# Kernel optimization log

Measured on AMD Instinct MI355X. Metric: run time of the kernel, lower is better.

The kernel has to match this reference:

```python
import jax, jax.numpy as jnp
import numpy as np

COST_CLASS = 1.0
COST_GIOU = 1.0
MAXV = 8  # max vertices of intersection of two convex quads


def _corners(box):  # (5,) -> (4,2) CCW corners of rotated box (cx,cy,w,h,theta)
    cx, cy, w, h, t = box[0], box[1], box[2], box[3], box[4]
    c, s = jnp.cos(t), jnp.sin(t)
    dx = jnp.array([-0.5, 0.5, 0.5, -0.5], box.dtype) * w
    dy = jnp.array([-0.5, -0.5, 0.5, 0.5], box.dtype) * h
    x = cx + dx * c - dy * s
    y = cy + dx * s + dy * c
    return jnp.stack([x, y], axis=-1)


def _poly_area(poly, cnt):  # shoelace on masked vertex buffer (MAXV,2)
    idx = jnp.arange(MAXV)
    valid = idx < cnt
    nxt = jnp.where(idx + 1 < cnt, idx + 1, 0)
    cr = poly[:, 0] * poly[nxt, 1] - poly[nxt, 0] * poly[:, 1]
    return 0.5 * jnp.abs(jnp.sum(jnp.where(valid, cr, 0.0)))


def _clip(carry, edge):  # Sutherland-Hodgman clip of masked polygon by halfplane left of edge a->b
    poly, cnt = carry
    a, b = edge[0], edge[1]
    d = b - a
    idx = jnp.arange(MAXV)
    valid = idx < cnt
    nxt_i = jnp.where(idx + 1 < cnt, idx + 1, 0)
    cur, nxt = poly, poly[nxt_i]
    s_cur = d[0] * (cur[:, 1] - a[1]) - d[1] * (cur[:, 0] - a[0])
    s_nxt = d[0] * (nxt[:, 1] - a[1]) - d[1] * (nxt[:, 0] - a[0])
    in_cur, in_nxt = s_cur >= 0, s_nxt >= 0
    den = s_cur - s_nxt
    den = jnp.where(jnp.abs(den) > 1e-9, den, 1e-9)
    ipt = cur + (s_cur / den)[:, None] * (nxt - cur)
    pts = jnp.stack([cur, ipt], 1).reshape(2 * MAXV, 2)
    msk = jnp.stack([valid & in_cur, valid & (in_cur ^ in_nxt)], 1).reshape(2 * MAXV)
    pos = jnp.where(msk, jnp.cumsum(msk) - 1, 2 * MAXV)
    new_poly = jnp.zeros((MAXV, 2), poly.dtype).at[pos].set(pts, mode='drop')
    return (new_poly, jnp.sum(msk).astype(cnt.dtype)), None


def _inter_area(cs, cc):  # intersection area of two convex quads (4,2),(4,2)
    poly0 = jnp.zeros((MAXV, 2), cs.dtype).at[:4].set(cs)
    edges = jnp.stack([cc, jnp.roll(cc, -1, axis=0)], axis=1)  # (4,2,2)
    (poly, cnt), _ = jax.lax.scan(_clip, (poly0, jnp.asarray(4, jnp.int32)), edges)
    return _poly_area(poly, cnt)


def _giou_cost(bt, bp):  # cal_giou(target, pred) ~= 1 - rotated GIoU
    ct, cp = _corners(bt), _corners(bp)
    inter = _inter_area(cp, ct)
    union = bt[2] * bt[3] + bp[2] * bp[3] - inter
    allc = jnp.concatenate([ct, cp], 0)
    enc = (allc[:, 0].max() - allc[:, 0].min()) * (allc[:, 1].max() - allc[:, 1].min())
    giou = inter / union - (enc - union) / enc
    return 1.0 - giou


def _costs(p_box, p_score, t_box, t_score):
    # p_box [B,M,5], t_box [B,N,5] with M >= N (m>n branch: zero-padded extra cols)
    B, M, _ = p_box.shape
    N = t_box.shape[1]
    box = jax.vmap(
        lambda pb, tb: jax.vmap(lambda bp: jax.vmap(lambda bt: _giou_cost(bt, bp))(tb))(pb)
    )(p_box, t_box)  # [B,M,N]
    score = jnp.maximum(0.0, t_score[:, None, :] - p_score[:, :, None])  # [B,M,N]
    pad = ((0, 0), (0, 0), (0, M - N))
    score_p = jnp.pad(score, pad)
    box_p = jnp.pad(box, pad)
    cost = COST_CLASS * score_p + COST_GIOU * box_p
    return cost, score_p, box_p

_costs_j = jax.jit(_costs)


def _lsa(cost):  # Hungarian (Jonker-Volgenant style, e-maxx), square cost matrix
    cost = np.asarray(cost, dtype=np.float64)
    n = cost.shape[0]
    INF = 1e30
    u = np.zeros(n + 1)
    v = np.zeros(n + 1)
    p = np.zeros(n + 1, dtype=np.int64)
    way = np.zeros(n + 1, dtype=np.int64)
    for i in range(1, n + 1):
        p[0] = i
        j0 = 0
        minv = np.full(n + 1, INF)
        used = np.zeros(n + 1, dtype=bool)
        while True:
            used[j0] = True
            i0 = p[j0]
            cur = cost[i0 - 1] - u[i0] - v[1:]
            free = ~used[1:]
            upd = free & (cur < minv[1:])
            minv[1:][upd] = cur[upd]
            way[1:][upd] = j0
            mv = np.where(free, minv[1:], INF)
            j0 = int(np.argmin(mv)) + 1
            delta = mv[j0 - 1]
            u[p[used]] += delta
            v[used] -= delta
            minv[1:][free] -= delta
            if p[j0] == 0:
                break
        while j0 != 0:
            j1 = way[j0]
            p[j0] = p[j1]
            j0 = j1
    cols = np.zeros(n, dtype=np.int64)
    for j in range(1, n + 1):
        cols[p[j] - 1] = j - 1
    return np.arange(n), cols


def setup_inputs() -> dict:
    key = jax.random.key(0)
    ks = jax.random.split(key, 6)
    B, M, N = 4, 256, 192

    def boxes(k1, k2, k3, n):
        c = jax.random.uniform(k1, (B, n, 2), minval=-50.0, maxval=50.0)
        wh = jax.random.uniform(k2, (B, n, 2), minval=1.0, maxval=5.0)
        ang = jax.random.uniform(k3, (B, n, 1), minval=-np.pi, maxval=np.pi)
        return jnp.concatenate([c, wh, ang], -1).astype(jnp.float32)

    return {
        'pred_rot_box': boxes(ks[0], ks[1], ks[2], M),
        'pred_score': jax.random.uniform(jax.random.fold_in(key, 10), (B, M), dtype=jnp.float32),
        'target_rot_box': boxes(ks[3], ks[4], ks[5], N),
        'target_score': jax.random.uniform(jax.random.fold_in(key, 11), (B, N), dtype=jnp.float32),
    }


def reference(pred_rot_box, pred_score, target_rot_box, target_score):
    cost, score_p, box_p = _costs_j(pred_rot_box, pred_score, target_rot_box, target_score)
    B = cost.shape[0]
    N = target_rot_box.shape[1]
    cost_np = np.asarray(cost)
    score_np = np.asarray(score_p)
    box_np = np.asarray(box_p)
    match, msc, mbc = [], [], []
    for b in range(B):
        r, c = _lsa(cost_np[b])
        match.append(cost_np[b][r, c].sum() / N)
        msc.append(score_np[b][r, c].sum() / N)
        mbc.append(box_np[b][r, c].sum() / N)
    return jnp.asarray(np.stack([match, msc, mbc]), dtype=jnp.float32)  # [3, B]
```

## Files before the change

### kernel.cpp

```cpp
#include <hip/hip_runtime.h>
#include <cmath>

#define MAXV 8

__global__ __launch_bounds__(256) void cost_kernel(
    const float* __restrict__ p_box, const float* __restrict__ p_score,
    const float* __restrict__ t_box, const float* __restrict__ t_score,
    float* __restrict__ Ct, float* __restrict__ boxc,
    int B, int M, int N)
{
    int g = blockIdx.x * 256 + threadIdx.x;
    int total = B * M * N;
    if (g >= total) return;
    int b = g / (M * N);
    int rem = g - b * M * N;
    int n = rem / M;
    int m = rem - n * M;

    const float* bp = p_box + ((size_t)b * M + m) * 5;
    const float* bt = t_box + ((size_t)b * N + n) * 5;
    float pcx = bp[0], pcy = bp[1], pw = bp[2], ph = bp[3], pth = bp[4];
    float tcx = bt[0], tcy = bt[1], tw = bt[2], th = bt[3], tth = bt[4];

    float pc = cosf(pth), ps = sinf(pth);
    float tc = cosf(tth), ts = sinf(tth);

    const float DX[4] = {-0.5f, 0.5f, 0.5f, -0.5f};
    const float DY[4] = {-0.5f, -0.5f, 0.5f, 0.5f};
    float cpx[4], cpy[4], ctx[4], cty[4];
#pragma unroll
    for (int k = 0; k < 4; k++) {
        float dx = DX[k] * pw, dy = DY[k] * ph;
        cpx[k] = pcx + dx * pc - dy * ps;
        cpy[k] = pcy + dx * ps + dy * pc;
        float dx2 = DX[k] * tw, dy2 = DY[k] * th;
        ctx[k] = tcx + dx2 * tc - dy2 * ts;
        cty[k] = tcy + dx2 * ts + dy2 * tc;
    }

    float px[MAXV], py[MAXV];
#pragma unroll
    for (int k = 0; k < MAXV; k++) {
        px[k] = (k < 4) ? cpx[k] : 0.0f;
        py[k] = (k < 4) ? cpy[k] : 0.0f;
    }
    int cnt = 4;

#pragma unroll
    for (int e = 0; e < 4; e++) {
        float ax = ctx[e], ay = cty[e];
        float bx2 = ctx[(e + 1) & 3], by2 = cty[(e + 1) & 3];
        float dx = bx2 - ax, dy = by2 - ay;
        float qx[MAXV], qy[MAXV];
#pragma unroll
        for (int k = 0; k < MAXV; k++) { qx[k] = 0.0f; qy[k] = 0.0f; }
        int nc = 0;
#pragma unroll
        for (int i = 0; i < MAXV; i++) {
            if (i < cnt) {
                bool wrap = !(i + 1 < cnt);
                float nx = wrap ? px[0] : px[(i + 1) & 7];
                float ny = wrap ? py[0] : py[(i + 1) & 7];
                float sc = dx * (py[i] - ay) - dy * (px[i] - ax);
                float sn = dx * (ny - ay) - dy * (nx - ax);
                bool inc = (sc >= 0.0f), inn = (sn >= 0.0f);
                float den = sc - sn;
                if (!(fabsf(den) > 1e-9f)) den = 1e-9f;
                float t = sc / den;
                float ix = px[i] + t * (nx - px[i]);
                float iy = py[i] + t * (ny - py[i]);
                if (inc) {
                    if (nc < MAXV) { qx[nc] = px[i]; qy[nc] = py[i]; }
                    nc++;
                }
                if (inc != inn) {
                    if (nc < MAXV) { qx[nc] = ix; qy[nc] = iy; }
                    nc++;
                }
            }
        }
        cnt = (nc > MAXV) ? MAXV : nc;
#pragma unroll
        for (int k = 0; k < MAXV; k++) {
            px[k] = (k < cnt) ? qx[k] : 0.0f;
            py[k] = (k < cnt) ? qy[k] : 0.0f;
        }
    }

    float a2 = 0.0f;
#pragma unroll
    for (int i = 0; i < MAXV; i++) {
        if (i < cnt) {
            bool wrap = !(i + 1 < cnt);
            float nx = wrap ? px[0] : px[(i + 1) & 7];
            float ny = wrap ? py[0] : py[(i + 1) & 7];
            a2 += px[i] * ny - nx * py[i];
        }
    }
    float inter = 0.5f * fabsf(a2);

    float uni = tw * th + pw * ph - inter;

    float xmin = ctx[0], xmax = ctx[0], ymin = cty[0], ymax = cty[0];
#pragma unroll
    for (int k = 1; k < 4; k++) {
        xmin = fminf(xmin, ctx[k]); xmax = fmaxf(xmax, ctx[k]);
        ymin = fminf(ymin, cty[k]); ymax = fmaxf(ymax, cty[k]);
    }
#pragma unroll
    for (int k = 0; k < 4; k++) {
        xmin = fminf(xmin, cpx[k]); xmax = fmaxf(xmax, cpx[k]);
        ymin = fminf(ymin, cpy[k]); ymax = fmaxf(ymax, cpy[k]);
    }
    float enc = (xmax - xmin) * (ymax - ymin);

    float giou = inter / uni - (enc - uni) / enc;
    float bc = 1.0f - giou;
    float scst = fmaxf(0.0f, t_score[b * N + n] - p_score[b * M + m]);

    Ct[((size_t)b * N + n) * M + m] = scst + bc;
    boxc[((size_t)b * M + m) * N + n] = bc;
}

__global__ __launch_bounds__(64) void rowmin_kernel(
    const float* __restrict__ Ct, float* __restrict__ rmv, int M)
{
    int bt = blockIdx.x;
    int lane = threadIdx.x;
    const float* row = Ct + (size_t)bt * M;

    float bv = 1e30f;
    for (int c = 4 * lane; c < M; c += 256) {
        float4 v = *reinterpret_cast<const float4*>(row + c);
        bv = fminf(bv, fminf(fminf(v.x, v.y), fminf(v.z, v.w)));
    }
#pragma unroll
    for (int off = 1; off < 64; off <<= 1)
        bv = fminf(bv, __shfl_xor(bv, off, 64));
    if (lane == 0) rmv[bt] = bv;
}

__global__ __launch_bounds__(256) void colmin_kernel(
    const float* __restrict__ Ct, const float* __restrict__ rmv,
    float* __restrict__ vmin, int* __restrict__ varg, int M, int N)
{
    int b = blockIdx.x;
    const float* Cb = Ct + (size_t)b * N * M;
    const float* rb = rmv + (size_t)b * N;
    for (int j = threadIdx.x; j < M; j += blockDim.x) {
        float bv = 1e30f; int bt = 0;
        for (int t = 0; t < N; ++t) {
            float val = Cb[(size_t)t * M + j] - rb[t];
            if (val < bv) { bv = val; bt = t; }
        }
        vmin[(size_t)b * M + j] = bv;
        varg[(size_t)b * M + j] = bt + 1;
    }
}

__device__ __forceinline__ int sel4(int a0, int a1, int a2, int a3, int s) {
    return s == 0 ? a0 : (s == 1 ? a1 : (s == 2 ? a2 : a3));
}

#define DPP_FMIN32_STAGE(val, CTRL) do {                                      \
    int _o = __builtin_amdgcn_update_dpp(0x7F800000,                          \
                 __float_as_int(val), CTRL, 0xf, 0xf, false);                 \
    (val) = fminf((val), __int_as_float(_o));                                 \
} while (0)

#define DPP_PAIR_STAGE(g1, g2, CTRL) do {                                     \
    int _b1 = __builtin_amdgcn_update_dpp(0x7F800000,                         \
                  __float_as_int(g1), CTRL, 0xf, 0xf, false);                 \
    int _b2 = __builtin_amdgcn_update_dpp(0x7F800000,                         \
                  __float_as_int(g2), CTRL, 0xf, 0xf, false);                 \
    float _o1 = __int_as_float(_b1), _o2 = __int_as_float(_b2);               \
    float _n2 = fminf(fmaxf((g1), _o1), fminf((g2), _o2));                    \
    (g1) = fminf((g1), _o1);                                                  \
    (g2) = _n2;                                                               \
} while (0)

__global__ __launch_bounds__(64) void hungarian_rect(
    const float* __restrict__ Ct, const float* __restrict__ boxc,
    const float* __restrict__ p_score, const float* __restrict__ t_score,
    const float* __restrict__ rmv, const float* __restrict__ vmin,
    const int* __restrict__ varg,
    float* __restrict__ out, int B, int M, int N)
{
    const float FINF = 1e30f;
    const int IINF = 0x7fffffff;
    int b = blockIdx.x;
    int lane = threadIdx.x;
    const float* C = Ct + (size_t)b * N * M;

    __shared__ float u[257];
    __shared__ int claim[257];
    __shared__ int ulist[257];
    __shared__ int dlist[257];

    {
        int total = N * M;
        for (int off = 4 * lane; off < total; off += 256) {
            float4 w = *reinterpret_cast<const float4*>(C + off);
            asm volatile("" :: "v"(w.x), "v"(w.y), "v"(w.z), "v"(w.w));
        }
    }

    for (int k = lane; k < N; k += 64) u[k + 1] = rmv[b * N + k];
    for (int k = lane; k < 257; k += 64) claim[k] = IINF;
    __syncthreads();

    const int j_base = 4 * lane + 1;
    float v0, v1, v2, v3;
    int va0, va1, va2, va3;
    {
        const float4 vm = *reinterpret_cast<const float4*>(
            vmin + (size_t)b * M + 4 * lane);
        v0 = vm.x; v1 = vm.y; v2 = vm.z; v3 = vm.w;
        const int4 vg = *reinterpret_cast<const int4*>(
            varg + (size_t)b * M + 4 * lane);
        va0 = vg.x; va1 = vg.y; va2 = vg.z; va3 = vg.w;
    }

    float m0, m1, m2, m3;
    int p0 = 0, p1 = 0, p2 = 0, p3 = 0;
    int w0 = 0, w1 = 0, w2 = 0, w3 = 0;

    atomicMin(&claim[va0], j_base + 0);
    atomicMin(&claim[va1], j_base + 1);
    atomicMin(&claim[va2], j_base + 2);
    atomicMin(&claim[va3], j_base + 3);
    __syncthreads();
    p0 = (claim[va0] == j_base + 0) ? va0 : 0;
    p1 = (claim[va1] == j_base + 1) ? va1 : 0;
    p2 = (claim[va2] == j_base + 2) ? va2 : 0;
    p3 = (claim[va3] == j_base + 3) ? va3 : 0;

    int ucnt = 0;
    for (int c0 = 0; c0 < N; c0 += 64) {
        int t = c0 + lane + 1;
        bool un = (t <= N) && (claim[t] == IINF);
        unsigned long long mask = __ballot(un);
        int pos = ucnt + __popcll(mask & ((1ULL << lane) - 1ULL));
        if (un) ulist[pos] = t;
        ucnt += (int)__popcll(mask);
    }
    __syncthreads();

    int dcnt = 0;
    {
        int pi = 0, steps = 0;
        int i = (pi < ucnt) ? ulist[pi++] : 0;
        while (i != 0) {
            ++steps;
            if (steps > 2048) {
                if (lane == 0) dlist[dcnt] = i;
                dcnt++;
                while (pi < ucnt) {
                    if (lane == 0) dlist[dcnt] = ulist[pi];
                    dcnt++; pi++;
                }
                break;
            }
            float4 r4 = *reinterpret_cast<const float4*>(
                C + (size_t)(i - 1) * M + 4 * lane);
            float rc0 = r4.x - v0, rc1 = r4.y - v1;
            float rc2 = r4.z - v2, rc3 = r4.w - v3;
            float l1 = rc0; int s1 = 0;
            if (rc1 < l1) { l1 = rc1; s1 = 1; }
            if (rc2 < l1) { l1 = rc2; s1 = 2; }
            if (rc3 < l1) { l1 = rc3; s1 = 3; }
            float l2 = FINF;
            if (s1 != 0) l2 = fminf(l2, rc0);
            if (s1 != 1) l2 = fminf(l2, rc1);
            if (s1 != 2) l2 = fminf(l2, rc2);
            if (s1 != 3) l2 = fminf(l2, rc3);

            float g1 = l1, g2 = l2;
            DPP_PAIR_STAGE(g1, g2, 0x111);
            DPP_PAIR_STAGE(g1, g2, 0x112);
            DPP_PAIR_STAGE(g1, g2, 0x114);
            DPP_PAIR_STAGE(g1, g2, 0x118);
            DPP_PAIR_STAGE(g1, g2, 0x142);
            DPP_PAIR_STAGE(g1, g2, 0x143);
            float u1 = __int_as_float(
                __builtin_amdgcn_readlane(__float_as_int(g1), 63));
            float u2 = __int_as_float(
                __builtin_amdgcn_readlane(__float_as_int(g2), 63));
            unsigned long long ball = __ballot(l1 == u1);
            int owner = __builtin_ctzll(ball);
            int pk = (j_base + s1) | (sel4(p0, p1, p2, p3, s1) << 9);
            pk = __builtin_amdgcn_readlane(pk, owner);
            int j1 = pk & 511, k = pk >> 9;

            if (u1 < u2) {
                if (lane == 0) u[i] = u2;
                if (lane == ((j1 - 1) >> 2)) {
                    int s = (j1 - 1) & 3;
                    float dv = u2 - u1;
                    if (s == 0) { v0 -= dv; p0 = i; }
                    else if (s == 1) { v1 -= dv; p1 = i; }
                    else if (s == 2) { v2 -= dv; p2 = i; }
                    else { v3 -= dv; p3 = i; }
                }
                if (k > 0) { i = k; continue; }
            } else if (k == 0) {
                if (lane == 0) u[i] = u1;
                if (lane == ((j1 - 1) >> 2)) {
                    int s = (j1 - 1) & 3;
                    if (s == 0) p0 = i;
                    else if (s == 1) p1 = i;
                    else if (s == 2) p2 = i;
                    else p3 = i;
                }
            } else {
                if (lane == 0) { u[i] = u1; dlist[dcnt] = i; }
                dcnt++;
            }
            i = (pi < ucnt) ? ulist[pi++] : 0;
        }
    }
    __syncthreads();

    for (int uk = 0; uk < dcnt; ++uk) {
        int t = dlist[uk];
        m0 = FINF; m1 = FINF; m2 = FINF; m3 = FINF;
        int usedm = 0;
        float ur0 = 0, ur1 = 0, ur2 = 0, ur3 = 0;
        int tg0 = 0, tg1 = 0, tg2 = 0, tg3 = 0;
        int j0 = 0;
        int icur = t;
        float ut = u[t];
        float u0 = ut;
        float4 r4 = *reinterpret_cast<const float4*>(
            C + (size_t)(t - 1) * M + 4 * lane);
        int jn;

        while (true) {
            if (j0 != 0 && ((j0 - 1) >> 2) == lane) {
                int s = (j0 - 1) & 3;
                usedm |= 1 << s;
                if (s == 0) { ur0 = u0; tg0 = icur; }
                else if (s == 1) { ur1 = u0; tg1 = icur; }
                else if (s == 2) { ur2 = u0; tg2 = icur; }
                else { ur3 = u0; tg3 = icur; }
            }

            float a0 = FINF, a1 = FINF, a2f = FINF, a3 = FINF;
            if (!(usedm & 1)) {
                float cur = (r4.x - u0) - v0;
                if (cur < m0) { m0 = cur; w0 = j0; }
                a0 = m0;
            }
            if (!(usedm & 2)) {
                float cur = (r4.y - u0) - v1;
                if (cur < m1) { m1 = cur; w1 = j0; }
                a1 = m1;
            }
            if (!(usedm & 4)) {
                float cur = (r4.z - u0) - v2;
                if (cur < m2) { m2 = cur; w2 = j0; }
                a2f = m2;
            }
            if (!(usedm & 8)) {
                float cur = (r4.w - u0) - v3;
                if (cur < m3) { m3 = cur; w3 = j0; }
                a3 = m3;
            }

            float av = a0; int sa = 0;
            if (a1 < av)  { av = a1;  sa = 1; }
            if (a2f < av) { av = a2f; sa = 2; }
            if (a3 < av)  { av = a3;  sa = 3; }

            float wv_ = av;
            DPP_FMIN32_STAGE(wv_, 0x111);
            DPP_FMIN32_STAGE(wv_, 0x112);
            DPP_FMIN32_STAGE(wv_, 0x114);
            DPP_FMIN32_STAGE(wv_, 0x118);
            DPP_FMIN32_STAGE(wv_, 0x142);
            DPP_FMIN32_STAGE(wv_, 0x143);
            float delta = __int_as_float(
                __builtin_amdgcn_readlane(__float_as_int(wv_), 63));

            unsigned long long ball = __ballot(av == delta);
            int owner = __builtin_ctzll(ball);
            int pk = (j_base + sa) | (sel4(p0, p1, p2, p3, sa) << 9);
            pk = __builtin_amdgcn_readlane(pk, owner);
            int jn_ = pk & 511, pjn = pk >> 9;

            int nxt = (pjn > 0) ? pjn : t;
            float u_next = u[nxt];
            float4 r4n = *reinterpret_cast<const float4*>(
                C + (size_t)(nxt - 1) * M + 4 * lane);

            if (usedm & 1) { ur0 += delta; v0 -= delta; } else m0 -= delta;
            if (usedm & 2) { ur1 += delta; v1 -= delta; } else m1 -= delta;
            if (usedm & 4) { ur2 += delta; v2 -= delta; } else m2 -= delta;
            if (usedm & 8) { ur3 += delta; v3 -= delta; } else m3 -= delta;
            ut += delta;

            jn = jn_;
            if (pjn == 0) break;
            j0 = jn_; u0 = u_next; r4 = r4n; icur = pjn;
        }

        if (usedm & 1) u[tg0] = ur0;
        if (usedm & 2) u[tg1] = ur1;
        if (usedm & 4) u[tg2] = ur2;
        if (usedm & 8) u[tg3] = ur3;
        if (lane == 0) u[t] = ut;

        int jj = jn, prev = 0;
        while (true) {
            int idx = jj - 1;
            int o = idx >> 2, s = idx & 3;
            int packv = sel4(w0, w1, w2, w3, s) |
                        (sel4(p0, p1, p2, p3, s) << 9);
            packv = __builtin_amdgcn_readlane(packv, o);
            int wv = packv & 511, pold = packv >> 9;
            if (prev != 0) {
                int pi = prev - 1;
                if (lane == (pi >> 2)) {
                    int sp = pi & 3;
                    if (sp == 0) p0 = pold;
                    else if (sp == 1) p1 = pold;
                    else if (sp == 2) p2 = pold;
                    else p3 = pold;
                }
            }
            if (wv == 0) {
                if (lane == o) {
                    if (s == 0) p0 = t;
                    else if (s == 1) p1 = t;
                    else if (s == 2) p2 = t;
                    else p3 = t;
                }
                break;
            }
            prev = jj; jj = wv;
        }
    }

    double sm = 0.0, ss = 0.0, sb = 0.0;
#pragma unroll
    for (int s = 0; s < 4; ++s) {
        int pt = sel4(p0, p1, p2, p3, s);
        if (pt != 0) {
            int r = j_base + s - 1;
            int c = pt - 1;
            sm += (double)C[(size_t)c * M + r];
            sb += (double)boxc[((size_t)b * M + r) * N + c];
            ss += (double)fmaxf(0.0f, t_score[b * N + c] - p_score[b * M + r]);
        }
    }
#pragma unroll
    for (int off = 1; off < 64; off <<= 1) {
        sm += __shfl_xor(sm, off, 64);
        ss += __shfl_xor(ss, off, 64);
        sb += __shfl_xor(sb, off, 64);
    }
    if (lane == 0) {
        out[0 * B + b] = (float)(sm / N);
        out[1 * B + b] = (float)(ss / N);
        out[2 * B + b] = (float)(sb / N);
    }
}

extern "C" void kernel_launch(void* const* d_in, const int* in_sizes, int n_in,
                              void* d_out, int out_size, void* d_ws, size_t ws_size,
                              hipStream_t stream) {
    int B = out_size / 3;
    int M = in_sizes[1] / B;
    int N = in_sizes[3] / B;

    const float* p_box   = (const float*)d_in[0];
    const float* p_score = (const float*)d_in[1];
    const float* t_box   = (const float*)d_in[2];
    const float* t_score = (const float*)d_in[3];
    float* out = (float*)d_out;

    float* Ct   = (float*)d_ws;
    float* boxc = Ct + (size_t)B * N * M;
    float* rmv  = boxc + (size_t)B * M * N;
    float* vmin = rmv + (size_t)B * N;
    int*   varg = (int*)(vmin + (size_t)B * M);

    int total = B * M * N;
    cost_kernel<<<(total + 255) / 256, 256, 0, stream>>>(
        p_box, p_score, t_box, t_score, Ct, boxc, B, M, N);
    rowmin_kernel<<<B * N, 64, 0, stream>>>(Ct, rmv, M);
    colmin_kernel<<<B, 256, 0, stream>>>(Ct, rmv, vmin, varg, M, N);
    hungarian_rect<<<B, 64, 0, stream>>>(
        Ct, boxc, p_score, t_score, rmv, vmin, varg, out, B, M, N);
}
```

Before: 230.2 us.

## Replace sequential augmenting row reduction with parallel auction-style bidding rounds

The serial augmenting row reduction in the Hungarian kernel, which handled one row per step using wave-wide DPP reductions, is replaced by up to 64 rounds of auction-style bidding. In each round every unassigned row scans its full cost row against prices held in LDS and finds its best and second-best columns. It then bids for its best column through a 64-bit atomicMax, and each winning column updates its owner and price. Each lane now reads whole rows serially instead of the wave cooperating on one row, which costs more memory traffic per row. The result could also differ from the old order and leave more rows for the later shortest-path augmentation phase.

```diff
diff --git a/kernel.cpp b/kernel.cpp
--- a/kernel.cpp
+++ b/kernel.cpp
@@ -168,17 +168,6 @@
     (val) = fminf((val), __int_as_float(_o));                                 \
 } while (0)
 
-#define DPP_PAIR_STAGE(g1, g2, CTRL) do {                                     \
-    int _b1 = __builtin_amdgcn_update_dpp(0x7F800000,                         \
-                  __float_as_int(g1), CTRL, 0xf, 0xf, false);                 \
-    int _b2 = __builtin_amdgcn_update_dpp(0x7F800000,                         \
-                  __float_as_int(g2), CTRL, 0xf, 0xf, false);                 \
-    float _o1 = __int_as_float(_b1), _o2 = __int_as_float(_b2);               \
-    float _n2 = fminf(fmaxf((g1), _o1), fminf((g2), _o2));                    \
-    (g1) = fminf((g1), _o1);                                                  \
-    (g2) = _n2;                                                               \
-} while (0)
-
 __global__ __launch_bounds__(64) void hungarian_rect(
     const float* __restrict__ Ct, const float* __restrict__ boxc,
     const float* __restrict__ p_score, const float* __restrict__ t_score,
@@ -193,8 +182,12 @@
     const float* C = Ct + (size_t)b * N * M;
 
     __shared__ float u[257];
+    __shared__ float v_lds[256];
+    __shared__ int colOwner[256];
+    __shared__ int rowMatch[257];
     __shared__ int claim[257];
-    __shared__ int ulist[257];
+    __shared__ unsigned long long bid[256];
+    __shared__ int rlist[257];
     __shared__ int dlist[257];
 
     {
@@ -206,120 +199,121 @@
     }
 
     for (int k = lane; k < N; k += 64) u[k + 1] = rmv[b * N + k];
-    for (int k = lane; k < 257; k += 64) claim[k] = IINF;
+    for (int k = lane; k < 257; k += 64) { claim[k] = IINF; rowMatch[k] = 0; }
     __syncthreads();
 
     const int j_base = 4 * lane + 1;
-    float v0, v1, v2, v3;
     int va0, va1, va2, va3;
     {
         const float4 vm = *reinterpret_cast<const float4*>(
             vmin + (size_t)b * M + 4 * lane);
-        v0 = vm.x; v1 = vm.y; v2 = vm.z; v3 = vm.w;
+        v_lds[4 * lane + 0] = vm.x; v_lds[4 * lane + 1] = vm.y;
+        v_lds[4 * lane + 2] = vm.z; v_lds[4 * lane + 3] = vm.w;
         const int4 vg = *reinterpret_cast<const int4*>(
             varg + (size_t)b * M + 4 * lane);
         va0 = vg.x; va1 = vg.y; va2 = vg.z; va3 = vg.w;
     }
-
-    float m0, m1, m2, m3;
-    int p0 = 0, p1 = 0, p2 = 0, p3 = 0;
-    int w0 = 0, w1 = 0, w2 = 0, w3 = 0;
 
     atomicMin(&claim[va0], j_base + 0);
     atomicMin(&claim[va1], j_base + 1);
     atomicMin(&claim[va2], j_base + 2);
     atomicMin(&claim[va3], j_base + 3);
     __syncthreads();
-    p0 = (claim[va0] == j_base + 0) ? va0 : 0;
-    p1 = (claim[va1] == j_base + 1) ? va1 : 0;
-    p2 = (claim[va2] == j_base + 2) ? va2 : 0;
-    p3 = (claim[va3] == j_base + 3) ? va3 : 0;
-
-    int ucnt = 0;
+    {
+        int own0 = (claim[va0] == j_base + 0) ? va0 : 0;
+        int own1 = (claim[va1] == j_base + 1) ? va1 : 0;
+        int own2 = (claim[va2] == j_base + 2) ? va2 : 0;
+        int own3 = (claim[va3] == j_base + 3) ? va3 : 0;
+        colOwner[4 * lane + 0] = own0; if (own0) rowMatch[own0] = j_base + 0;
+        colOwner[4 * lane + 1] = own1; if (own1) rowMatch[own1] = j_base + 1;
+        colOwner[4 * lane + 2] = own2; if (own2) rowMatch[own2] = j_base + 2;
+        colOwner[4 * lane + 3] = own3; if (own3) rowMatch[own3] = j_base + 3;
+    }
+    __syncthreads();
+
+    for (int round = 0; round < 64; ++round) {
+        int rcnt = 0;
+        for (int c0 = 0; c0 < N; c0 += 64) {
+            int t = c0 + lane + 1;
+            bool un = (t <= N) && (rowMatch[t] == 0);
+            unsigned long long mask = __ballot(un);
+            int pos = rcnt + (int)__popcll(mask & ((1ULL << lane) - 1ULL));
+            if (un) rlist[pos] = t;
+            rcnt += (int)__popcll(mask);
+        }
+        if (rcnt == 0) break;
+        for (int j = lane; j < M; j += 64) bid[j] = 0ULL;
+        __syncthreads();
+
+        for (int c0 = 0; c0 < rcnt; c0 += 64) {
+            int t = (c0 + lane < rcnt) ? rlist[c0 + lane] : 0;
+            if (t) {
+                const float* row = C + (size_t)(t - 1) * M;
+                float mn1 = FINF, mn2 = FINF; int j1 = 0;
+                for (int jj = 0; jj < M; jj += 4) {
+                    float4 c4 = *reinterpret_cast<const float4*>(row + jj);
+                    float rc;
+                    rc = c4.x - v_lds[jj];
+                    if (rc < mn1) { mn2 = mn1; mn1 = rc; j1 = jj; }
+                    else mn2 = fminf(mn2, rc);
+                    rc = c4.y - v_lds[jj + 1];
+                    if (rc < mn1) { mn2 = mn1; mn1 = rc; j1 = jj + 1; }
+                    else mn2 = fminf(mn2, rc);
+                    rc = c4.z - v_lds[jj + 2];
+                    if (rc < mn1) { mn2 = mn1; mn1 = rc; j1 = jj + 2; }
+                    else mn2 = fminf(mn2, rc);
+                    rc = c4.w - v_lds[jj + 3];
+                    if (rc < mn1) { mn2 = mn1; mn1 = rc; j1 = jj + 3; }
+                    else mn2 = fminf(mn2, rc);
+                }
+                float dv = mn2 - mn1;
+                if (dv == 0.0f && colOwner[j1] != 0) {
+                    rowMatch[t] = -1;
+                } else {
+                    u[t] = mn2;
+                    unsigned long long pk =
+                        ((unsigned long long)(unsigned)__float_as_int(dv) << 32)
+                        | (unsigned)t;
+                    atomicMax(&bid[j1], pk);
+                }
+            }
+        }
+        __syncthreads();
+
+#pragma unroll
+        for (int s = 0; s < 4; ++s) {
+            int j = 4 * lane + s;
+            unsigned long long bk = bid[j];
+            if (bk) {
+                int r = (int)(unsigned)(bk & 0xffffffffULL);
+                float dv = __int_as_float((int)(bk >> 32));
+                int old = colOwner[j];
+                colOwner[j] = r;
+                rowMatch[r] = j + 1;
+                if (old) rowMatch[old] = 0;
+                v_lds[j] -= dv;
+            }
+        }
+        __syncthreads();
+    }
+
+    int dcnt = 0;
     for (int c0 = 0; c0 < N; c0 += 64) {
         int t = c0 + lane + 1;
-        bool un = (t <= N) && (claim[t] == IINF);
-        unsigned long long mask = __ballot(un);
-        int pos = ucnt + __popcll(mask & ((1ULL << lane) - 1ULL));
-        if (un) ulist[pos] = t;
-        ucnt += (int)__popcll(mask);
+        bool dd = (t <= N) && (rowMatch[t] <= 0);
+        unsigned long long mask = __ballot(dd);
+        int pos = dcnt + (int)__popcll(mask & ((1ULL << lane) - 1ULL));
+        if (dd) dlist[pos] = t;
+        dcnt += (int)__popcll(mask);
     }
     __syncthreads();
 
-    int dcnt = 0;
-    {
-        int pi = 0, steps = 0;
-        int i = (pi < ucnt) ? ulist[pi++] : 0;
-        while (i != 0) {
-            ++steps;
-            if (steps > 2048) {
-                if (lane == 0) dlist[dcnt] = i;
-                dcnt++;
-                while (pi < ucnt) {
-                    if (lane == 0) dlist[dcnt] = ulist[pi];
-                    dcnt++; pi++;
-                }
-                break;
-            }
-            float4 r4 = *reinterpret_cast<const float4*>(
-                C + (size_t)(i - 1) * M + 4 * lane);
-            float rc0 = r4.x - v0, rc1 = r4.y - v1;
-            float rc2 = r4.z - v2, rc3 = r4.w - v3;
-            float l1 = rc0; int s1 = 0;
-            if (rc1 < l1) { l1 = rc1; s1 = 1; }
-            if (rc2 < l1) { l1 = rc2; s1 = 2; }
-            if (rc3 < l1) { l1 = rc3; s1 = 3; }
-            float l2 = FINF;
-            if (s1 != 0) l2 = fminf(l2, rc0);
-            if (s1 != 1) l2 = fminf(l2, rc1);
-            if (s1 != 2) l2 = fminf(l2, rc2);
-            if (s1 != 3) l2 = fminf(l2, rc3);
-
-            float g1 = l1, g2 = l2;
-            DPP_PAIR_STAGE(g1, g2, 0x111);
-            DPP_PAIR_STAGE(g1, g2, 0x112);
-            DPP_PAIR_STAGE(g1, g2, 0x114);
-            DPP_PAIR_STAGE(g1, g2, 0x118);
-            DPP_PAIR_STAGE(g1, g2, 0x142);
-            DPP_PAIR_STAGE(g1, g2, 0x143);
-            float u1 = __int_as_float(
-                __builtin_amdgcn_readlane(__float_as_int(g1), 63));
-            float u2 = __int_as_float(
-                __builtin_amdgcn_readlane(__float_as_int(g2), 63));
-            unsigned long long ball = __ballot(l1 == u1);
-            int owner = __builtin_ctzll(ball);
-            int pk = (j_base + s1) | (sel4(p0, p1, p2, p3, s1) << 9);
-            pk = __builtin_amdgcn_readlane(pk, owner);
-            int j1 = pk & 511, k = pk >> 9;
-
-            if (u1 < u2) {
-                if (lane == 0) u[i] = u2;
-                if (lane == ((j1 - 1) >> 2)) {
-                    int s = (j1 - 1) & 3;
-                    float dv = u2 - u1;
-                    if (s == 0) { v0 -= dv; p0 = i; }
-                    else if (s == 1) { v1 -= dv; p1 = i; }
-                    else if (s == 2) { v2 -= dv; p2 = i; }
-                    else { v3 -= dv; p3 = i; }
-                }
-                if (k > 0) { i = k; continue; }
-            } else if (k == 0) {
-                if (lane == 0) u[i] = u1;
-                if (lane == ((j1 - 1) >> 2)) {
-                    int s = (j1 - 1) & 3;
-                    if (s == 0) p0 = i;
-                    else if (s == 1) p1 = i;
-                    else if (s == 2) p2 = i;
-                    else p3 = i;
-                }
-            } else {
-                if (lane == 0) { u[i] = u1; dlist[dcnt] = i; }
-                dcnt++;
-            }
-            i = (pi < ucnt) ? ulist[pi++] : 0;
-        }
-    }
-    __syncthreads();
+    float v0 = v_lds[4 * lane + 0], v1 = v_lds[4 * lane + 1];
+    float v2 = v_lds[4 * lane + 2], v3 = v_lds[4 * lane + 3];
+    int p0 = colOwner[4 * lane + 0], p1 = colOwner[4 * lane + 1];
+    int p2 = colOwner[4 * lane + 2], p3 = colOwner[4 * lane + 3];
+    int w0 = 0, w1 = 0, w2 = 0, w3 = 0;
+    float m0, m1, m2, m3;
 
     for (int uk = 0; uk < dcnt; ++uk) {
         int t = dlist[uk];
```

Result: slower. 622.0 us (+170.2%).

## Switch Hungarian duals to double and add reduction-transfer and zero-delta auction steps

Applied to the files above, without the earlier changes.

Moves the dual potentials, column minima and warp reductions in the Hungarian solver from float to double, using split 32-bit DPP moves for the 64-bit min reductions. After the initial column-claim assignment it adds a reduction-transfer step that tightens the duals of assigned rows. It also lets the greedy augmenting phase take a few extra zero-slack reassignment steps per row, so fewer rows fall through to the expensive shortest-path loop. The FP64 arithmetic and doubled DPP traffic make each step of the serial loop costlier, and the rmv pointer cast to double may be misaligned for odd sizes.

```diff
diff --git a/kernel.cpp b/kernel.cpp
--- a/kernel.cpp
+++ b/kernel.cpp
@@ -142,15 +142,15 @@
 
 __global__ __launch_bounds__(256) void colmin_kernel(
     const float* __restrict__ Ct, const float* __restrict__ rmv,
-    float* __restrict__ vmin, int* __restrict__ varg, int M, int N)
+    double* __restrict__ vmin, int* __restrict__ varg, int M, int N)
 {
     int b = blockIdx.x;
     const float* Cb = Ct + (size_t)b * N * M;
     const float* rb = rmv + (size_t)b * N;
     for (int j = threadIdx.x; j < M; j += blockDim.x) {
-        float bv = 1e30f; int bt = 0;
+        double bv = 1e30; int bt = 0;
         for (int t = 0; t < N; ++t) {
-            float val = Cb[(size_t)t * M + j] - rb[t];
+            double val = (double)Cb[(size_t)t * M + j] - (double)rb[t];
             if (val < bv) { bv = val; bt = t; }
         }
         vmin[(size_t)b * M + j] = bv;
@@ -162,40 +162,60 @@
     return s == 0 ? a0 : (s == 1 ? a1 : (s == 2 ? a2 : a3));
 }
 
-#define DPP_FMIN32_STAGE(val, CTRL) do {                                      \
-    int _o = __builtin_amdgcn_update_dpp(0x7F800000,                          \
-                 __float_as_int(val), CTRL, 0xf, 0xf, false);                 \
-    (val) = fminf((val), __int_as_float(_o));                                 \
+#define DPP_FMIN64_STAGE(val, CTRL) do {                                      \
+    long long _bits = __double_as_longlong(val);                              \
+    int _lo = __builtin_amdgcn_update_dpp(0, (int)_bits,                      \
+                                          CTRL, 0xf, 0xf, false);             \
+    int _hi = __builtin_amdgcn_update_dpp(0x7FF00000, (int)(_bits >> 32),     \
+                                          CTRL, 0xf, 0xf, false);             \
+    double _o = __longlong_as_double(                                         \
+        ((long long)_hi << 32) | (unsigned)_lo);                              \
+    (val) = fmin((val), _o);                                                  \
 } while (0)
 
-#define DPP_PAIR_STAGE(g1, g2, CTRL) do {                                     \
-    int _b1 = __builtin_amdgcn_update_dpp(0x7F800000,                         \
-                  __float_as_int(g1), CTRL, 0xf, 0xf, false);                 \
-    int _b2 = __builtin_amdgcn_update_dpp(0x7F800000,                         \
-                  __float_as_int(g2), CTRL, 0xf, 0xf, false);                 \
-    float _o1 = __int_as_float(_b1), _o2 = __int_as_float(_b2);               \
-    float _n2 = fminf(fmaxf((g1), _o1), fminf((g2), _o2));                    \
-    (g1) = fminf((g1), _o1);                                                  \
+#define DPP_PAIR64_STAGE(g1, g2, CTRL) do {                                   \
+    long long _b1 = __double_as_longlong(g1);                                 \
+    long long _b2 = __double_as_longlong(g2);                                 \
+    int _l1 = __builtin_amdgcn_update_dpp(0, (int)_b1, CTRL, 0xf, 0xf, false);\
+    int _h1 = __builtin_amdgcn_update_dpp(0x7FF00000, (int)(_b1 >> 32),       \
+                                          CTRL, 0xf, 0xf, false);             \
+    int _l2 = __builtin_amdgcn_update_dpp(0, (int)_b2, CTRL, 0xf, 0xf, false);\
+    int _h2 = __builtin_amdgcn_update_dpp(0x7FF00000, (int)(_b2 >> 32),       \
+                                          CTRL, 0xf, 0xf, false);             \
+    double _o1 = __longlong_as_double(((long long)_h1 << 32) | (unsigned)_l1);\
+    double _o2 = __longlong_as_double(((long long)_h2 << 32) | (unsigned)_l2);\
+    double _n2 = fmin(fmax((g1), _o1), fmin((g2), _o2));                      \
+    (g1) = fmin((g1), _o1);                                                   \
     (g2) = _n2;                                                               \
 } while (0)
+
+__device__ __forceinline__ double readlane_f64(double v, int lane) {
+    long long b = __double_as_longlong(v);
+    int lo = __builtin_amdgcn_readlane((int)b, lane);
+    int hi = __builtin_amdgcn_readlane((int)(b >> 32), lane);
+    return __longlong_as_double(((long long)hi << 32) | (unsigned)lo);
+}
 
 __global__ __launch_bounds__(64) void hungarian_rect(
     const float* __restrict__ Ct, const float* __restrict__ boxc,
     const float* __restrict__ p_score, const float* __restrict__ t_score,
-    const float* __restrict__ rmv, const float* __restrict__ vmin,
+    const float* __restrict__ rmv, const double* __restrict__ vmin,
     const int* __restrict__ varg,
     float* __restrict__ out, int B, int M, int N)
 {
-    const float FINF = 1e30f;
+    const double DINF = 1e30;
     const int IINF = 0x7fffffff;
     int b = blockIdx.x;
     int lane = threadIdx.x;
     const float* C = Ct + (size_t)b * N * M;
 
-    __shared__ float u[257];
+    __shared__ double u[257];
+    __shared__ double v_lds[256];
+    __shared__ double tmin[257];
     __shared__ int claim[257];
     __shared__ int ulist[257];
     __shared__ int dlist[257];
+    __shared__ int zcnt[257];
 
     {
         int total = N * M;
@@ -205,23 +225,24 @@
         }
     }
 
-    for (int k = lane; k < N; k += 64) u[k + 1] = rmv[b * N + k];
-    for (int k = lane; k < 257; k += 64) claim[k] = IINF;
-    __syncthreads();
+    for (int k = lane; k < N; k += 64) u[k + 1] = (double)rmv[b * N + k];
+    for (int k = lane; k < 257; k += 64) { claim[k] = IINF; zcnt[k] = 0; }
 
     const int j_base = 4 * lane + 1;
-    float v0, v1, v2, v3;
+    double v0, v1, v2, v3;
     int va0, va1, va2, va3;
     {
-        const float4 vm = *reinterpret_cast<const float4*>(
-            vmin + (size_t)b * M + 4 * lane);
-        v0 = vm.x; v1 = vm.y; v2 = vm.z; v3 = vm.w;
+        const double* vb = vmin + (size_t)b * M + 4 * lane;
+        v0 = vb[0]; v1 = vb[1]; v2 = vb[2]; v3 = vb[3];
+        v_lds[4 * lane + 0] = v0; v_lds[4 * lane + 1] = v1;
+        v_lds[4 * lane + 2] = v2; v_lds[4 * lane + 3] = v3;
         const int4 vg = *reinterpret_cast<const int4*>(
             varg + (size_t)b * M + 4 * lane);
         va0 = vg.x; va1 = vg.y; va2 = vg.z; va3 = vg.w;
     }
-
-    float m0, m1, m2, m3;
+    __syncthreads();
+
+    double m0, m1, m2, m3;
     int p0 = 0, p1 = 0, p2 = 0, p3 = 0;
     int w0 = 0, w1 = 0, w2 = 0, w3 = 0;
 
@@ -234,17 +255,60 @@
     p1 = (claim[va1] == j_base + 1) ? va1 : 0;
     p2 = (claim[va2] == j_base + 2) ? va2 : 0;
     p3 = (claim[va3] == j_base + 3) ? va3 : 0;
+
+    __syncthreads();
+    for (int k = lane; k < 257; k += 64) claim[k] = IINF;
+    __syncthreads();
+    if (p0) claim[p0] = j_base + 0;
+    if (p1) claim[p1] = j_base + 1;
+    if (p2) claim[p2] = j_base + 2;
+    if (p3) claim[p3] = j_base + 3;
+    __syncthreads();
 
     int ucnt = 0;
     for (int c0 = 0; c0 < N; c0 += 64) {
         int t = c0 + lane + 1;
         bool un = (t <= N) && (claim[t] == IINF);
         unsigned long long mask = __ballot(un);
-        int pos = ucnt + __popcll(mask & ((1ULL << lane) - 1ULL));
+        int pos = ucnt + (int)__popcll(mask & ((1ULL << lane) - 1ULL));
         if (un) ulist[pos] = t;
         ucnt += (int)__popcll(mask);
     }
     __syncthreads();
+
+    for (int c0 = 0; c0 < N; c0 += 64) {
+        int t = c0 + lane + 1;
+        if (t <= N && claim[t] != IINF) {
+            int jt = claim[t] - 1;
+            const float* row = C + (size_t)(t - 1) * M;
+            double mn = DINF;
+            for (int jj = 0; jj < M; jj += 4) {
+                float4 c4 = *reinterpret_cast<const float4*>(row + jj);
+                double r0 = (double)c4.x - v_lds[jj];
+                double r1 = (double)c4.y - v_lds[jj + 1];
+                double r2 = (double)c4.z - v_lds[jj + 2];
+                double r3 = (double)c4.w - v_lds[jj + 3];
+                if (jj     != jt) mn = fmin(mn, r0);
+                if (jj + 1 != jt) mn = fmin(mn, r1);
+                if (jj + 2 != jt) mn = fmin(mn, r2);
+                if (jj + 3 != jt) mn = fmin(mn, r3);
+            }
+            tmin[t] = mn;
+        }
+    }
+    __syncthreads();
+    for (int c0 = 0; c0 < N; c0 += 64) {
+        int t = c0 + lane + 1;
+        if (t <= N && claim[t] != IINF) {
+            double mn = tmin[t];
+            double dv = fmax(mn - u[t], 0.0);
+            u[t] = mn;
+            v_lds[claim[t] - 1] -= dv;
+        }
+    }
+    __syncthreads();
+    v0 = v_lds[4 * lane + 0]; v1 = v_lds[4 * lane + 1];
+    v2 = v_lds[4 * lane + 2]; v3 = v_lds[4 * lane + 3];
 
     int dcnt = 0;
     {
@@ -263,29 +327,27 @@
             }
             float4 r4 = *reinterpret_cast<const float4*>(
                 C + (size_t)(i - 1) * M + 4 * lane);
-            float rc0 = r4.x - v0, rc1 = r4.y - v1;
-            float rc2 = r4.z - v2, rc3 = r4.w - v3;
-            float l1 = rc0; int s1 = 0;
+            double rc0 = (double)r4.x - v0, rc1 = (double)r4.y - v1;
+            double rc2 = (double)r4.z - v2, rc3 = (double)r4.w - v3;
+            double l1 = rc0; int s1 = 0;
             if (rc1 < l1) { l1 = rc1; s1 = 1; }
             if (rc2 < l1) { l1 = rc2; s1 = 2; }
             if (rc3 < l1) { l1 = rc3; s1 = 3; }
-            float l2 = FINF;
-            if (s1 != 0) l2 = fminf(l2, rc0);
-            if (s1 != 1) l2 = fminf(l2, rc1);
-            if (s1 != 2) l2 = fminf(l2, rc2);
-            if (s1 != 3) l2 = fminf(l2, rc3);
-
-            float g1 = l1, g2 = l2;
-            DPP_PAIR_STAGE(g1, g2, 0x111);
-            DPP_PAIR_STAGE(g1, g2, 0x112);
-            DPP_PAIR_STAGE(g1, g2, 0x114);
-            DPP_PAIR_STAGE(g1, g2, 0x118);
-            DPP_PAIR_STAGE(g1, g2, 0x142);
-            DPP_PAIR_STAGE(g1, g2, 0x143);
-            float u1 = __int_as_float(
-                __builtin_amdgcn_readlane(__float_as_int(g1), 63));
-            float u2 = __int_as_float(
-                __builtin_amdgcn_readlane(__float_as_int(g2), 63));
+            double l2 = DINF;
+            if (s1 != 0) l2 = fmin(l2, rc0);
+            if (s1 != 1) l2 = fmin(l2, rc1);
+            if (s1 != 2) l2 = fmin(l2, rc2);
+            if (s1 != 3) l2 = fmin(l2, rc3);
+
+            double g1 = l1, g2 = l2;
+            DPP_PAIR64_STAGE(g1, g2, 0x111);
+            DPP_PAIR64_STAGE(g1, g2, 0x112);
+            DPP_PAIR64_STAGE(g1, g2, 0x114);
+            DPP_PAIR64_STAGE(g1, g2, 0x118);
+            DPP_PAIR64_STAGE(g1, g2, 0x142);
+            DPP_PAIR64_STAGE(g1, g2, 0x143);
+            double u1 = readlane_f64(g1, 63);
+            double u2 = readlane_f64(g2, 63);
             unsigned long long ball = __ballot(l1 == u1);
             int owner = __builtin_ctzll(ball);
             int pk = (j_base + s1) | (sel4(p0, p1, p2, p3, s1) << 9);
@@ -296,7 +358,7 @@
                 if (lane == 0) u[i] = u2;
                 if (lane == ((j1 - 1) >> 2)) {
                     int s = (j1 - 1) & 3;
-                    float dv = u2 - u1;
+                    double dv = u2 - u1;
                     if (s == 0) { v0 -= dv; p0 = i; }
                     else if (s == 1) { v1 -= dv; p1 = i; }
                     else if (s == 2) { v2 -= dv; p2 = i; }
@@ -312,6 +374,16 @@
                     else if (s == 2) p2 = i;
                     else p3 = i;
                 }
+            } else if (zcnt[i] < 4) {
+                if (lane == 0) { zcnt[i] = zcnt[i] + 1; u[i] = u1; }
+                if (lane == ((j1 - 1) >> 2)) {
+                    int s = (j1 - 1) & 3;
+                    if (s == 0) p0 = i;
+                    else if (s == 1) p1 = i;
+                    else if (s == 2) p2 = i;
+                    else p3 = i;
+                }
+                i = k; continue;
             } else {
                 if (lane == 0) { u[i] = u1; dlist[dcnt] = i; }
                 dcnt++;
@@ -323,14 +395,14 @@
 
     for (int uk = 0; uk < dcnt; ++uk) {
         int t = dlist[uk];
-        m0 = FINF; m1 = FINF; m2 = FINF; m3 = FINF;
+        m0 = DINF; m1 = DINF; m2 = DINF; m3 = DINF;
         int usedm = 0;
-        float ur0 = 0, ur1 = 0, ur2 = 0, ur3 = 0;
+        double ur0 = 0, ur1 = 0, ur2 = 0, ur3 = 0;
         int tg0 = 0, tg1 = 0, tg2 = 0, tg3 = 0;
         int j0 = 0;
         int icur = t;
-        float ut = u[t];
-        float u0 = ut;
+        double ut = u[t];
+        double u0 = ut;
         float4 r4 = *reinterpret_cast<const float4*>(
             C + (size_t)(t - 1) * M + 4 * lane);
         int jn;
@@ -345,42 +417,41 @@
                 else { ur3 = u0; tg3 = icur; }
             }
 
-            float a0 = FINF, a1 = FINF, a2f = FINF, a3 = FINF;
+            double a0 = DINF, a1 = DINF, a2d = DINF, a3 = DINF;
             if (!(usedm & 1)) {
-                float cur = (r4.x - u0) - v0;
+                double cur = ((double)r4.x - u0) - v0;
                 if (cur < m0) { m0 = cur; w0 = j0; }
                 a0 = m0;
             }
             if (!(usedm & 2)) {
-                float cur = (r4.y - u0) - v1;
+                double cur = ((double)r4.y - u0) - v1;
                 if (cur < m1) { m1 = cur; w1 = j0; }
                 a1 = m1;
             }
             if (!(usedm & 4)) {
-                float cur = (r4.z - u0) - v2;
+                double cur = ((double)r4.z - u0) - v2;
                 if (cur < m2) { m2 = cur; w2 = j0; }
-                a2f = m2;
+                a2d = m2;
             }
             if (!(usedm & 8)) {
-                float cur = (r4.w - u0) - v3;
+                double cur = ((double)r4.w - u0) - v3;
                 if (cur < m3) { m3 = cur; w3 = j0; }
                 a3 = m3;
             }
 
-            float av = a0; int sa = 0;
+            double av = a0; int sa = 0;
             if (a1 < av)  { av = a1;  sa = 1; }
-            if (a2f < av) { av = a2f; sa = 2; }
+            if (a2d < av) { av = a2d; sa = 2; }
             if (a3 < av)  { av = a3;  sa = 3; }
 
-            float wv_ = av;
-            DPP_FMIN32_STAGE(wv_, 0x111);
-            DPP_FMIN32_STAGE(wv_, 0x112);
-            DPP_FMIN32_STAGE(wv_, 0x114);
-            DPP_FMIN32_STAGE(wv_, 0x118);
-            DPP_FMIN32_STAGE(wv_, 0x142);
-            DPP_FMIN32_STAGE(wv_, 0x143);
-            float delta = __int_as_float(
-                __builtin_amdgcn_readlane(__float_as_int(wv_), 63));
+            double wv_ = av;
+            DPP_FMIN64_STAGE(wv_, 0x111);
+            DPP_FMIN64_STAGE(wv_, 0x112);
+            DPP_FMIN64_STAGE(wv_, 0x114);
+            DPP_FMIN64_STAGE(wv_, 0x118);
+            DPP_FMIN64_STAGE(wv_, 0x142);
+            DPP_FMIN64_STAGE(wv_, 0x143);
+            double delta = readlane_f64(wv_, 63);
 
             unsigned long long ball = __ballot(av == delta);
             int owner = __builtin_ctzll(ball);
@@ -389,7 +460,7 @@
             int jn_ = pk & 511, pjn = pk >> 9;
 
             int nxt = (pjn > 0) ? pjn : t;
-            float u_next = u[nxt];
+            double u_next = u[nxt];
             float4 r4n = *reinterpret_cast<const float4*>(
                 C + (size_t)(nxt - 1) * M + 4 * lane);
 
@@ -479,11 +550,11 @@
     const float* t_score = (const float*)d_in[3];
     float* out = (float*)d_out;
 
-    float* Ct   = (float*)d_ws;
-    float* boxc = Ct + (size_t)B * N * M;
-    float* rmv  = boxc + (size_t)B * M * N;
-    float* vmin = rmv + (size_t)B * N;
-    int*   varg = (int*)(vmin + (size_t)B * M);
+    float*  Ct   = (float*)d_ws;
+    float*  boxc = Ct + (size_t)B * N * M;
+    float*  rmv  = boxc + (size_t)B * M * N;
+    double* vmin = (double*)(rmv + (size_t)B * N);
+    int*    varg = (int*)(vmin + (size_t)B * M);
 
     int total = B * M * N;
     cost_kernel<<<(total + 255) / 256, 256, 0, stream>>>(
```

After: 261.2 us. 1.13x slower.
